# Optimization experiments

Measured on AMD Instinct MI355X. Metric: run time of the kernel, lower is better.

## Reference

```python
import jax, jax.numpy as jnp
import numpy as np

HIDDEN = 2048
NUM_HEADS = 16
HEAD_DIM = 128
BLOCK_SIZE = 64
NUM_ACTIVE_BLOCKS = 4  # diagonal pattern -> bandwidth = 2 blocks each side
NEG_INF = -1e30  # stand-in for -inf that is safe under softmax in fp32


def _block_diagonal_additive_mask(seq_len: int) -> jnp.ndarray:
    """Token-level additive mask [S, S]; 0 where block |bi-bj|<=bandwidth, -inf else."""
    bandwidth = NUM_ACTIVE_BLOCKS // 2
    bid = jnp.arange(seq_len) // BLOCK_SIZE  # [S]
    active = jnp.abs(bid[:, None] - bid[None, :]) <= bandwidth  # [S, S] bool
    return jnp.where(active, 0.0, NEG_INF).astype(jnp.float32)


def setup_inputs() -> dict:
    key = jax.random.key(0)
    k0, k1, k2, k3, k4 = jax.random.split(key, 5)
    B, S = 2, 2048
    scale = 1.0 / np.sqrt(HIDDEN)
    return {
        "hidden_states": jax.random.normal(k0, (B, S, HIDDEN), dtype=jnp.float32),
        "Wq": jax.random.normal(k1, (HIDDEN, NUM_HEADS * HEAD_DIM), dtype=jnp.float32) * scale,
        "Wk": jax.random.normal(k2, (HIDDEN, NUM_HEADS * HEAD_DIM), dtype=jnp.float32) * scale,
        "Wv": jax.random.normal(k3, (HIDDEN, NUM_HEADS * HEAD_DIM), dtype=jnp.float32) * scale,
        "Wo": jax.random.normal(k4, (NUM_HEADS * HEAD_DIM, HIDDEN), dtype=jnp.float32) * scale,
    }


def reference(hidden_states, Wq, Wk, Wv, Wo):
    B, S, _ = hidden_states.shape
    scaling = HEAD_DIM ** -0.5

    # projections -> [B, H, S, D]
    def split_heads(x):
        return x.reshape(B, S, NUM_HEADS, HEAD_DIM).transpose(0, 2, 1, 3)

    q = split_heads(hidden_states @ Wq)
    k = split_heads(hidden_states @ Wk)
    v = split_heads(hidden_states @ Wv)

    mask = _block_diagonal_additive_mask(S)  # [S, S]

    # scores [B, H, S, S]
    scores = jnp.einsum("bhsd,bhtd->bhst", q, k) * scaling + mask[None, None]
    attn = jax.nn.softmax(scores.astype(jnp.float32), axis=-1).astype(q.dtype)

    out = jnp.einsum("bhst,bhtd->bhsd", attn, v)  # [B, H, S, D]
    out = out.transpose(0, 2, 1, 3).reshape(B, S, NUM_HEADS * HEAD_DIM)
    return out @ Wo
```

## Files before the change

### kernel.cpp

```cpp
#include <hip/hip_runtime.h>

typedef __attribute__((ext_vector_type(4))) float f32x4;
typedef __attribute__((ext_vector_type(8))) _Float16 f16x8;
typedef __attribute__((ext_vector_type(4))) _Float16 f16x4;

__device__ __forceinline__ void gload_lds16(const void* g, void* l) {
  __builtin_amdgcn_global_load_lds((__attribute__((address_space(1))) void*)(g),
                                   (__attribute__((address_space(3))) void*)(l), 16, 0, 0);
}

__global__ __launch_bounds__(256) void cast_f32_f16(const float* __restrict__ x,
                                                    _Float16* __restrict__ y, int n) {
  int i = (blockIdx.x * 256 + threadIdx.x) * 4;
  if (i < n) {
    float4 v = *(const float4*)(x + i);
    f16x4 o = { (_Float16)v.x, (_Float16)v.y, (_Float16)v.z, (_Float16)v.w };
    *(f16x4*)(y + i) = o;
  }
}

__global__ __launch_bounds__(256) void wtrans(const float* __restrict__ W0, const float* __restrict__ W1,
                                              const float* __restrict__ W2, const float* __restrict__ W3,
                                              _Float16* __restrict__ out) {
  const float* W = blockIdx.z == 0 ? W0 : blockIdx.z == 1 ? W1 : blockIdx.z == 2 ? W2 : W3;
  _Float16* Wt = out + (size_t)blockIdx.z * (2048u * 2048u);
  __shared__ _Float16 tile[64][65];
  const int tid = threadIdx.x;
  const int k0 = blockIdx.y * 64, n0 = blockIdx.x * 64;
  #pragma unroll
  for (int p = 0; p < 4; ++p) {
    int o = p * 256 + tid, r = o >> 4, c = o & 15;
    float4 v = *(const float4*)(W + (size_t)(k0 + r) * 2048 + n0 + c * 4);
    tile[r][c * 4 + 0] = (_Float16)v.x;
    tile[r][c * 4 + 1] = (_Float16)v.y;
    tile[r][c * 4 + 2] = (_Float16)v.z;
    tile[r][c * 4 + 3] = (_Float16)v.w;
  }
  __syncthreads();
  #pragma unroll
  for (int p = 0; p < 2; ++p) {
    int o = p * 256 + tid, nl = o >> 3, c = o & 7;
    f16x8 u;
    #pragma unroll
    for (int i = 0; i < 8; ++i) u[i] = tile[c * 8 + i][nl];
    *(f16x8*)(Wt + (size_t)(n0 + nl) * 2048 + k0 + c * 8) = u;
  }
}

__global__ __launch_bounds__(256) void vtrans(const _Float16* __restrict__ V, _Float16* __restrict__ Vt) {
  const int s0 = blockIdx.x * 64, d0 = blockIdx.y * 64, bh = blockIdx.z;
  const int b = bh >> 4, h = bh & 15;
  __shared__ _Float16 tile[64][65];
  const int tid = threadIdx.x;
  #pragma unroll
  for (int p = 0; p < 2; ++p) {
    int o = p * 256 + tid, sl = o >> 3, c = o & 7;
    f16x8 v = *(const f16x8*)(V + (size_t)(b * 2048 + s0 + sl) * 2048 + h * 128 + d0 + c * 8);
    #pragma unroll
    for (int i = 0; i < 8; ++i) tile[sl][c * 8 + i] = v[i];
  }
  __syncthreads();
  #pragma unroll
  for (int p = 0; p < 2; ++p) {
    int o = p * 256 + tid, dl = o >> 3, c = o & 7;
    f16x8 u;
    #pragma unroll
    for (int i = 0; i < 8; ++i) u[i] = tile[c * 8 + i][dl];
    *(f16x8*)(Vt + (size_t)(bh * 128 + d0 + dl) * 2048 + s0 + c * 8) = u;
  }
}

template <typename OutT>
__global__ __launch_bounds__(256) void gemm_bt(const _Float16* __restrict__ A,
                                               const _Float16* __restrict__ Bt,
                                               OutT* __restrict__ C,
                                               int K, int N, size_t zsB, size_t zsC) {
  Bt += (size_t)blockIdx.z * zsB;
  C  += (size_t)blockIdx.z * zsC;
  __shared__ _Float16 As[128 * 32];
  __shared__ _Float16 Bs[128 * 32];
  const int tid = threadIdx.x;
  const int m0 = blockIdx.y * 128, n0 = blockIdx.x * 128;
  const int lane = tid & 63, w = tid >> 6, l16 = lane & 15, quad = lane >> 4;
  const int wm = (w & 1) * 64, wn = (w >> 1) * 64;
  f32x4 acc[4][4];
  #pragma unroll
  for (int i = 0; i < 4; ++i)
    #pragma unroll
    for (int j = 0; j < 4; ++j) acc[i][j] = (f32x4){0.f, 0.f, 0.f, 0.f};

  const int r0 = tid >> 2;
  const int c0 = ((tid & 3) ^ ((r0 >> 1) & 3)) * 8;
  const int swz = (quad ^ ((l16 >> 1) & 3)) * 8;

  for (int k0 = 0; k0 < K; k0 += 32) {
    __syncthreads();
    #pragma unroll
    for (int p = 0; p < 2; ++p) {
      int r = p * 64 + r0;
      gload_lds16(A  + (size_t)(m0 + r) * K + k0 + c0, (char*)As + (p * 256 + tid) * 16);
      gload_lds16(Bt + (size_t)(n0 + r) * K + k0 + c0, (char*)Bs + (p * 256 + tid) * 16);
    }
    __builtin_amdgcn_s_waitcnt(0);
    __syncthreads();
    f16x8 af[4], bfv[4];
    #pragma unroll
    for (int i = 0; i < 4; ++i) af[i]  = *(const f16x8*)(As + (wm + i * 16 + l16) * 32 + swz);
    #pragma unroll
    for (int j = 0; j < 4; ++j) bfv[j] = *(const f16x8*)(Bs + (wn + j * 16 + l16) * 32 + swz);
    #pragma unroll
    for (int i = 0; i < 4; ++i)
      #pragma unroll
      for (int j = 0; j < 4; ++j)
        acc[i][j] = __builtin_amdgcn_mfma_f32_16x16x32_f16(bfv[j], af[i], acc[i][j], 0, 0, 0);
  }
  #pragma unroll
  for (int i = 0; i < 4; ++i) {
    const size_t row = (size_t)(m0 + wm + i * 16 + l16);
    #pragma unroll
    for (int j = 0; j < 4; ++j) {
      const int col = n0 + wn + j * 16 + quad * 4;
      if constexpr (sizeof(OutT) == 2) {
        f16x4 o = { (_Float16)acc[i][j][0], (_Float16)acc[i][j][1],
                    (_Float16)acc[i][j][2], (_Float16)acc[i][j][3] };
        *(f16x4*)((_Float16*)C + row * N + col) = o;
      } else {
        *(f32x4*)((float*)C + row * N + col) = acc[i][j];
      }
    }
  }
}

__global__ __launch_bounds__(256) void attn(const _Float16* __restrict__ Qg,
                                            const _Float16* __restrict__ Kg,
                                            const _Float16* __restrict__ Vtg,
                                            _Float16* __restrict__ Og) {
  const int t = blockIdx.x, h = blockIdx.y, b = blockIdx.z;
  __shared__ _Float16 Qs[128 * 128];
  __shared__ _Float16 Ks[64 * 128];
  __shared__ _Float16 Vs[128 * 64];
  const int tid = threadIdx.x;
  const int lane = tid & 63, w = tid >> 6, l16 = lane & 15, quad = lane >> 4;
  const int qbw = 2 * t + (w >> 1);
  const char* QsB = (const char*)Qs;
  const char* KsB = (const char*)Ks;
  const char* VsB = (const char*)Vs;

  #pragma unroll
  for (int p = 0; p < 8; ++p) {
    int o = p * 256 + tid, r = o >> 4, c = o & 15;
    gload_lds16(Qg + (size_t)(b * 2048 + t * 128 + r) * 2048 + h * 128 + ((c ^ (r & 15)) * 8),
                (char*)Qs + o * 16);
  }
  __builtin_amdgcn_s_waitcnt(0);
  __syncthreads();
  f16x8 qf[2][4];
  #pragma unroll
  for (int qc = 0; qc < 2; ++qc)
    #pragma unroll
    for (int ks = 0; ks < 4; ++ks)
      qf[qc][ks] = *(const f16x8*)(QsB + (w * 32 + qc * 16 + l16) * 256 +
                                   (((ks * 4 + quad) ^ l16) * 16));

  const float scale = 0.08838834764831845f;
  float m_[2] = {-1e30f, -1e30f}, l_[2] = {0.f, 0.f};
  f32x4 oacc[8][2];
  #pragma unroll
  for (int dt = 0; dt < 8; ++dt)
    #pragma unroll
    for (int qc = 0; qc < 2; ++qc) oacc[dt][qc] = (f32x4){0.f, 0.f, 0.f, 0.f};

  for (int jj = 0; jj < 6; ++jj) {
    const int j = 2 * t - 2 + jj;
    const int jc = j < 0 ? 0 : (j > 31 ? 31 : j);
    __syncthreads();
    #pragma unroll
    for (int p = 0; p < 4; ++p) {
      int o = p * 256 + tid, r = o >> 4, c = o & 15;
      gload_lds16(Kg + (size_t)(b * 2048 + jc * 64 + r) * 2048 + h * 128 + ((c ^ (r & 15)) * 8),
                  (char*)Ks + o * 16);
    }
    #pragma unroll
    for (int p = 0; p < 4; ++p) {
      int o = p * 256 + tid, d = o >> 3, c = o & 7;
      gload_lds16(Vtg + (size_t)((b * 16 + h) * 128 + d) * 2048 + jc * 64 + ((c ^ (d & 7)) * 8),
                  (char*)Vs + o * 16);
    }
    __builtin_amdgcn_s_waitcnt(0);
    __syncthreads();

    const bool valid = (j >= 0) && (j <= 31) && (j >= qbw - 2) && (j <= qbw + 2);
    if (valid) {
      f32x4 sc[4][2];
      #pragma unroll
      for (int kt = 0; kt < 4; ++kt)
        #pragma unroll
        for (int qc = 0; qc < 2; ++qc) sc[kt][qc] = (f32x4){0.f, 0.f, 0.f, 0.f};
      #pragma unroll
      for (int kt = 0; kt < 4; ++kt)
        #pragma unroll
        for (int ks = 0; ks < 4; ++ks) {
          f16x8 kf = *(const f16x8*)(KsB + (kt * 16 + l16) * 256 + (((ks * 4 + quad) ^ l16) * 16));
          #pragma unroll
          for (int qc = 0; qc < 2; ++qc)
            sc[kt][qc] = __builtin_amdgcn_mfma_f32_16x16x32_f16(kf, qf[qc][ks], sc[kt][qc], 0, 0, 0);
        }
      #pragma unroll
      for (int qc = 0; qc < 2; ++qc) {
        float mj = -1e30f;
        #pragma unroll
        for (int kt = 0; kt < 4; ++kt)
          #pragma unroll
          for (int r = 0; r < 4; ++r) {
            float v = sc[kt][qc][r] * scale;
            sc[kt][qc][r] = v;
            mj = fmaxf(mj, v);
          }
        mj = fmaxf(mj, __shfl_xor(mj, 16));
        mj = fmaxf(mj, __shfl_xor(mj, 32));
        const float mn = fmaxf(m_[qc], mj);
        const float alpha = __expf(m_[qc] - mn);
        float s_ = 0.f;
        #pragma unroll
        for (int kt = 0; kt < 4; ++kt)
          #pragma unroll
          for (int r = 0; r < 4; ++r) {
            float p = __expf(sc[kt][qc][r] - mn);
            sc[kt][qc][r] = p;
            s_ += p;
          }
        s_ += __shfl_xor(s_, 16);
        s_ += __shfl_xor(s_, 32);
        l_[qc] = l_[qc] * alpha + s_;
        m_[qc] = mn;
        #pragma unroll
        for (int dt = 0; dt < 8; ++dt) oacc[dt][qc] *= alpha;
      }
      #pragma unroll
      for (int kt = 0; kt < 4; ++kt) {
        f16x4 pb[2];
        #pragma unroll
        for (int qc = 0; qc < 2; ++qc)
          pb[qc] = (f16x4){ (_Float16)sc[kt][qc][0], (_Float16)sc[kt][qc][1],
                            (_Float16)sc[kt][qc][2], (_Float16)sc[kt][qc][3] };
        #pragma unroll
        for (int dt = 0; dt < 8; ++dt) {
          f16x4 vv = *(const f16x4*)(VsB + (dt * 16 + l16) * 128 +
                                     (((2 * kt + (quad >> 1)) ^ (l16 & 7)) * 16) + (quad & 1) * 8);
          #pragma unroll
          for (int qc = 0; qc < 2; ++qc)
            oacc[dt][qc] = __builtin_amdgcn_mfma_f32_16x16x16f16(vv, pb[qc], oacc[dt][qc], 0, 0, 0);
        }
      }
    }
  }

  #pragma unroll
  for (int qc = 0; qc < 2; ++qc) {
    const float pinv = 1.0f / l_[qc];
    const size_t orow = (size_t)(b * 2048 + t * 128 + w * 32 + qc * 16 + l16);
    #pragma unroll
    for (int dt = 0; dt < 8; ++dt) {
      f16x4 ov = { (_Float16)(oacc[dt][qc][0] * pinv), (_Float16)(oacc[dt][qc][1] * pinv),
                   (_Float16)(oacc[dt][qc][2] * pinv), (_Float16)(oacc[dt][qc][3] * pinv) };
      *(f16x4*)(Og + orow * 2048 + h * 128 + dt * 16 + quad * 4) = ov;
    }
  }
}

extern "C" void kernel_launch(void* const* d_in, const int* in_sizes, int n_in,
                              void* d_out, int out_size, void* d_ws, size_t ws_size,
                              hipStream_t stream) {
  const float* Hs = (const float*)d_in[0];
  const float* Wq = (const float*)d_in[1];
  const float* Wk = (const float*)d_in[2];
  const float* Wv = (const float*)d_in[3];
  const float* Wo = (const float*)d_in[4];
  _Float16* Hb  = (_Float16*)d_ws;
  _Float16* Wt  = Hb  + 8388608;
  _Float16* Qb  = Wt  + 16777216;
  _Float16* Kb  = Qb  + 8388608;
  _Float16* Vb  = Kb  + 8388608;
  _Float16* Vtb = Vb  + 8388608;
  _Float16* Ob  = Vtb + 8388608;
  float* out = (float*)d_out;

  cast_f32_f16<<<8192, 256, 0, stream>>>(Hs, Hb, 8388608);
  wtrans<<<dim3(32, 32, 4), 256, 0, stream>>>(Wq, Wk, Wv, Wo, Wt);
  gemm_bt<_Float16><<<dim3(16, 32, 3), 256, 0, stream>>>(Hb, Wt, Qb, 2048, 2048,
                                                         (size_t)4194304, (size_t)8388608);
  vtrans<<<dim3(32, 2, 32), 256, 0, stream>>>(Vb, Vtb);
  attn<<<dim3(16, 16, 2), 256, 0, stream>>>(Qb, Kb, Vtb, Ob);
  gemm_bt<float><<<dim3(16, 32, 1), 256, 0, stream>>>(Ob, Wt + 3 * 4194304, out, 2048, 2048,
                                                      (size_t)0, (size_t)0);
}
```

Baseline: 388.3 us.

## Use 32x32x16 MFMA with BK=64 in GEMM; compute V transposed directly

The GEMM kernel now uses 32x32x16 MFMA tiles with a 64-wide K step and an XOR-swizzled LDS layout. This halves the number of K-loop barriers and reduces LDS fragment reads per MFMA. The V projection is computed as Wv^T times H^T, so it writes V already transposed and the separate vtrans kernel plus one workspace buffer are removed. The risks are higher LDS use per block and a changed Vt indexing in the attention kernel.

```diff
diff --git a/kernel.cpp b/kernel.cpp
--- a/kernel.cpp
+++ b/kernel.cpp
@@ -1,6 +1,7 @@
 #include <hip/hip_runtime.h>
 
 typedef __attribute__((ext_vector_type(4))) float f32x4;
+typedef __attribute__((ext_vector_type(16))) float f32x16;
 typedef __attribute__((ext_vector_type(8))) _Float16 f16x8;
 typedef __attribute__((ext_vector_type(4))) _Float16 f16x4;
 
@@ -47,29 +48,6 @@
   }
 }
 
-__global__ __launch_bounds__(256) void vtrans(const _Float16* __restrict__ V, _Float16* __restrict__ Vt) {
-  const int s0 = blockIdx.x * 64, d0 = blockIdx.y * 64, bh = blockIdx.z;
-  const int b = bh >> 4, h = bh & 15;
-  __shared__ _Float16 tile[64][65];
-  const int tid = threadIdx.x;
-  #pragma unroll
-  for (int p = 0; p < 2; ++p) {
-    int o = p * 256 + tid, sl = o >> 3, c = o & 7;
-    f16x8 v = *(const f16x8*)(V + (size_t)(b * 2048 + s0 + sl) * 2048 + h * 128 + d0 + c * 8);
-    #pragma unroll
-    for (int i = 0; i < 8; ++i) tile[sl][c * 8 + i] = v[i];
-  }
-  __syncthreads();
-  #pragma unroll
-  for (int p = 0; p < 2; ++p) {
-    int o = p * 256 + tid, dl = o >> 3, c = o & 7;
-    f16x8 u;
-    #pragma unroll
-    for (int i = 0; i < 8; ++i) u[i] = tile[c * 8 + i][dl];
-    *(f16x8*)(Vt + (size_t)(bh * 128 + d0 + dl) * 2048 + s0 + c * 8) = u;
-  }
-}
-
 template <typename OutT>
 __global__ __launch_bounds__(256) void gemm_bt(const _Float16* __restrict__ A,
                                                const _Float16* __restrict__ Bt,
@@ -77,55 +55,62 @@
                                                int K, int N, size_t zsB, size_t zsC) {
   Bt += (size_t)blockIdx.z * zsB;
   C  += (size_t)blockIdx.z * zsC;
-  __shared__ _Float16 As[128 * 32];
-  __shared__ _Float16 Bs[128 * 32];
+  __shared__ _Float16 As[128 * 64];
+  __shared__ _Float16 Bs[128 * 64];
   const int tid = threadIdx.x;
   const int m0 = blockIdx.y * 128, n0 = blockIdx.x * 128;
-  const int lane = tid & 63, w = tid >> 6, l16 = lane & 15, quad = lane >> 4;
+  const int lane = tid & 63, w = tid >> 6, l32 = lane & 31, half = lane >> 5;
   const int wm = (w & 1) * 64, wn = (w >> 1) * 64;
-  f32x4 acc[4][4];
-  #pragma unroll
-  for (int i = 0; i < 4; ++i)
-    #pragma unroll
-    for (int j = 0; j < 4; ++j) acc[i][j] = (f32x4){0.f, 0.f, 0.f, 0.f};
-
-  const int r0 = tid >> 2;
-  const int c0 = ((tid & 3) ^ ((r0 >> 1) & 3)) * 8;
-  const int swz = (quad ^ ((l16 >> 1) & 3)) * 8;
-
-  for (int k0 = 0; k0 < K; k0 += 32) {
-    __syncthreads();
-    #pragma unroll
-    for (int p = 0; p < 2; ++p) {
-      int r = p * 64 + r0;
-      gload_lds16(A  + (size_t)(m0 + r) * K + k0 + c0, (char*)As + (p * 256 + tid) * 16);
-      gload_lds16(Bt + (size_t)(n0 + r) * K + k0 + c0, (char*)Bs + (p * 256 + tid) * 16);
+  f32x16 acc[2][2];
+  #pragma unroll
+  for (int i = 0; i < 2; ++i)
+    #pragma unroll
+    for (int j = 0; j < 2; ++j) acc[i][j] = 0;
+
+  for (int k0 = 0; k0 < K; k0 += 64) {
+    __syncthreads();
+    #pragma unroll
+    for (int p = 0; p < 4; ++p) {
+      int o = p * 256 + tid, r = o >> 3, c = o & 7;
+      int cs = ((c ^ (r & 7)) * 8);
+      gload_lds16(A  + (size_t)(m0 + r) * K + k0 + cs, (char*)As + o * 16);
+      gload_lds16(Bt + (size_t)(n0 + r) * K + k0 + cs, (char*)Bs + o * 16);
     }
     __builtin_amdgcn_s_waitcnt(0);
     __syncthreads();
-    f16x8 af[4], bfv[4];
-    #pragma unroll
-    for (int i = 0; i < 4; ++i) af[i]  = *(const f16x8*)(As + (wm + i * 16 + l16) * 32 + swz);
-    #pragma unroll
-    for (int j = 0; j < 4; ++j) bfv[j] = *(const f16x8*)(Bs + (wn + j * 16 + l16) * 32 + swz);
-    #pragma unroll
-    for (int i = 0; i < 4; ++i)
-      #pragma unroll
-      for (int j = 0; j < 4; ++j)
-        acc[i][j] = __builtin_amdgcn_mfma_f32_16x16x32_f16(bfv[j], af[i], acc[i][j], 0, 0, 0);
-  }
-  #pragma unroll
-  for (int i = 0; i < 4; ++i) {
-    const size_t row = (size_t)(m0 + wm + i * 16 + l16);
-    #pragma unroll
-    for (int j = 0; j < 4; ++j) {
-      const int col = n0 + wn + j * 16 + quad * 4;
-      if constexpr (sizeof(OutT) == 2) {
-        f16x4 o = { (_Float16)acc[i][j][0], (_Float16)acc[i][j][1],
-                    (_Float16)acc[i][j][2], (_Float16)acc[i][j][3] };
-        *(f16x4*)((_Float16*)C + row * N + col) = o;
-      } else {
-        *(f32x4*)((float*)C + row * N + col) = acc[i][j];
+    #pragma unroll
+    for (int kk = 0; kk < 4; ++kk) {
+      const int slot = ((2 * kk + half) ^ (l32 & 7)) * 8;
+      f16x8 af[2], bf[2];
+      #pragma unroll
+      for (int s = 0; s < 2; ++s) {
+        af[s] = *(const f16x8*)(As + (wm + s * 32 + l32) * 64 + slot);
+        bf[s] = *(const f16x8*)(Bs + (wn + s * 32 + l32) * 64 + slot);
+      }
+      #pragma unroll
+      for (int sm = 0; sm < 2; ++sm)
+        #pragma unroll
+        for (int sn = 0; sn < 2; ++sn)
+          acc[sm][sn] = __builtin_amdgcn_mfma_f32_32x32x16_f16(bf[sn], af[sm], acc[sm][sn], 0, 0, 0);
+    }
+  }
+  #pragma unroll
+  for (int sm = 0; sm < 2; ++sm) {
+    const size_t row = (size_t)(m0 + wm + sm * 32 + l32);
+    #pragma unroll
+    for (int sn = 0; sn < 2; ++sn) {
+      #pragma unroll
+      for (int g = 0; g < 4; ++g) {
+        const int col = n0 + wn + sn * 32 + g * 8 + 4 * half;
+        if constexpr (sizeof(OutT) == 2) {
+          f16x4 o = { (_Float16)acc[sm][sn][4 * g + 0], (_Float16)acc[sm][sn][4 * g + 1],
+                      (_Float16)acc[sm][sn][4 * g + 2], (_Float16)acc[sm][sn][4 * g + 3] };
+          *(f16x4*)((_Float16*)C + row * N + col) = o;
+        } else {
+          f32x4 o = { acc[sm][sn][4 * g + 0], acc[sm][sn][4 * g + 1],
+                      acc[sm][sn][4 * g + 2], acc[sm][sn][4 * g + 3] };
+          *(f32x4*)((float*)C + row * N + col) = o;
+        }
       }
     }
   }
@@ -183,7 +168,7 @@
     #pragma unroll
     for (int p = 0; p < 4; ++p) {
       int o = p * 256 + tid, d = o >> 3, c = o & 7;
-      gload_lds16(Vtg + (size_t)((b * 16 + h) * 128 + d) * 2048 + jc * 64 + ((c ^ (d & 7)) * 8),
+      gload_lds16(Vtg + (size_t)(h * 128 + d) * 4096 + b * 2048 + jc * 64 + ((c ^ (d & 7)) * 8),
                   (char*)Vs + o * 16);
     }
     __builtin_amdgcn_s_waitcnt(0);
@@ -280,16 +265,16 @@
   _Float16* Wt  = Hb  + 8388608;
   _Float16* Qb  = Wt  + 16777216;
   _Float16* Kb  = Qb  + 8388608;
-  _Float16* Vb  = Kb  + 8388608;
-  _Float16* Vtb = Vb  + 8388608;
+  _Float16* Vtb = Kb  + 8388608;
   _Float16* Ob  = Vtb + 8388608;
   float* out = (float*)d_out;
 
   cast_f32_f16<<<8192, 256, 0, stream>>>(Hs, Hb, 8388608);
   wtrans<<<dim3(32, 32, 4), 256, 0, stream>>>(Wq, Wk, Wv, Wo, Wt);
-  gemm_bt<_Float16><<<dim3(16, 32, 3), 256, 0, stream>>>(Hb, Wt, Qb, 2048, 2048,
+  gemm_bt<_Float16><<<dim3(16, 32, 2), 256, 0, stream>>>(Hb, Wt, Qb, 2048, 2048,
                                                          (size_t)4194304, (size_t)8388608);
-  vtrans<<<dim3(32, 2, 32), 256, 0, stream>>>(Vb, Vtb);
+  gemm_bt<_Float16><<<dim3(32, 16, 1), 256, 0, stream>>>(Wt + 2 * 4194304, Hb, Vtb, 2048, 4096,
+                                                         (size_t)0, (size_t)0);
   attn<<<dim3(16, 16, 2), 256, 0, stream>>>(Qb, Kb, Vtb, Ob);
   gemm_bt<float><<<dim3(16, 32, 1), 256, 0, stream>>>(Ob, Wt + 3 * 4194304, out, 2048, 2048,
                                                       (size_t)0, (size_t)0);
```

New measurement: 363.8 us. 6.3% less time.
